# Optimization experiments

Measured on AMD Instinct MI355X. Metric: run time of the kernel, lower is better.

## Reference

```python
import jax, jax.numpy as jnp
import numpy as np

B, T, J, E, H = 32, 120, 24, 128, 8
d = E // H           # attention_dim = 16
D = J * E            # input_dim = 3072
FF = 256
NEG = -1e9


def _bn(x, g, b):
    # BatchNorm1d over channels-last layout: normalize each of D channels over (batch, time)
    m = x.mean(axis=(0, 1))
    v = x.var(axis=(0, 1))
    return (x - m) * jax.lax.rsqrt(v + 1e-5) * g + b


def setup_inputs() -> dict:
    key = jax.random.key(0)
    ks = jax.random.split(key, 12)
    s = 0.05  # keep activations well-scaled
    return {
        "src_seqs": jax.random.normal(ks[0], (B, T, D), jnp.float32),
        "Wq_t": jax.random.normal(ks[1], (H, J, d, E), jnp.float32) * s,
        "Wk_t": jax.random.normal(ks[2], (H, J, d, E), jnp.float32) * s,
        "Wv_t": jax.random.normal(ks[3], (H, J, d, E), jnp.float32) * s,
        "Wp_t": jax.random.normal(ks[4], (D, D), jnp.float32) * s,
        "bp_t": jnp.zeros((D,), jnp.float32),
        "g_t": jnp.ones((D,), jnp.float32),
        "b_t": jnp.zeros((D,), jnp.float32),
        "Wq_s": jax.random.normal(ks[5], (H, J, d, E), jnp.float32) * s,
        "Wk_s": jax.random.normal(ks[6], (H, d, E), jnp.float32) * s,
        "Wv_s": jax.random.normal(ks[7], (H, d, E), jnp.float32) * s,
        "Wp_s": jax.random.normal(ks[8], (D, D), jnp.float32) * s,
        "bp_s": jnp.zeros((D,), jnp.float32),
        "g_s": jnp.ones((D,), jnp.float32),
        "b_s": jnp.zeros((D,), jnp.float32),
        "W1": jax.random.normal(ks[9], (FF, D), jnp.float32) * s,
        "b1": jnp.zeros((FF,), jnp.float32),
        "W2": jax.random.normal(ks[10], (D, FF), jnp.float32) * s,
        "b2": jnp.zeros((D,), jnp.float32),
        "g_f": jnp.ones((D,), jnp.float32),
        "b_f": jnp.zeros((D,), jnp.float32),
    }


def reference(src_seqs, Wq_t, Wk_t, Wv_t, Wp_t, bp_t, g_t, b_t,
              Wq_s, Wk_s, Wv_s, Wp_s, bp_s, g_s, b_s,
              W1, b1, W2, b2, g_f, b_f):
    Bz, Tz, Dz = src_seqs.shape
    x = src_seqs.reshape(Bz, Tz, J, E)  # per-joint embeddings
    sc = 1.0 / jnp.sqrt(jnp.float32(d))

    # ---- temporal attention (per head h, per joint j; causal over time) ----
    q = jnp.einsum('btje,hjde->bhjtd', x, Wq_t)
    k = jnp.einsum('btje,hjde->bhjtd', x, Wk_t)
    v = jnp.einsum('btje,hjde->bhjtd', x, Wv_t)
    causal = jnp.where(jnp.tril(jnp.ones((Tz, Tz), bool)), 0.0, NEG)
    a = jax.nn.softmax(jnp.einsum('bhjtd,bhjsd->bhjts', q, k) * sc + causal, axis=-1)
    ta = jnp.einsum('bhjts,bhjsd->bhjtd', a, v)
    # concat order: heads outer, joints inner -> (b,t,h,j,d)
    ta = ta.transpose(0, 3, 1, 2, 4).reshape(Bz, Tz, Dz)
    ta = ta @ Wp_t.T + bp_t
    ta = _bn(ta + src_seqs, g_t, b_t)  # dropout=identity (eval)

    # ---- spatial attention (per head h; attends over joints, shared K/V proj) ----
    qs = jnp.einsum('btje,hjde->bhtjd', x, Wq_s)
    ks = jnp.einsum('btje,hde->bhtjd', x, Wk_s)
    vs = jnp.einsum('btje,hde->bhtjd', x, Wv_s)
    asft = jax.nn.softmax(jnp.einsum('bhtjd,bhtkd->bhtjk', qs, ks) * sc, axis=-1)
    sa = jnp.einsum('bhtjk,bhtkd->bhtjd', asft, vs)
    sa = sa.transpose(0, 2, 1, 3, 4).reshape(Bz, Tz, Dz)  # (b,t,h,j,d)
    sa = sa @ Wp_s.T + bp_s
    sa = _bn(sa + src_seqs, g_s, b_s)

    # ---- feed-forward + residual + norm ----
    att = ta + sa
    h1 = jax.nn.relu(att @ W1.T + b1)
    out = _bn((h1 @ W2.T + b2) + att, g_f, b_f)
    return out
```

## Files before the change

### kernel.cpp

```cpp
#include <hip/hip_runtime.h>

typedef unsigned short u16;
typedef __bf16 bf16x8 __attribute__((ext_vector_type(8)));
typedef float f4 __attribute__((ext_vector_type(4)));
typedef float float4v __attribute__((ext_vector_type(4)));
typedef u16 u16x4 __attribute__((ext_vector_type(4)));

#define NX 11796480
#define LDP 136

__device__ __forceinline__ float bf2f(u16 u){ __bf16 h = __builtin_bit_cast(__bf16, u); return (float)h; }
__device__ __forceinline__ u16 f2bf(float f){ __bf16 h = (__bf16)f; return __builtin_bit_cast(u16, h); }

__device__ __forceinline__ void gload_lds16(const u16* g, u16* l){
  __builtin_amdgcn_global_load_lds((const __attribute__((address_space(1))) void*)g,
                                   (__attribute__((address_space(3))) void*)l, 16, 0, 0);
}

__device__ __forceinline__ void cvt4seg(const float* __restrict__ in, u16* __restrict__ out, int i){
  float4v v = *(const float4v*)&in[i*4];
  u16x4 o;
  o[0]=f2bf(v[0]); o[1]=f2bf(v[1]); o[2]=f2bf(v[2]); o[3]=f2bf(v[3]);
  *(u16x4*)&out[i*4] = o;
}

__global__ void k_prep(const float* __restrict__ src, u16* __restrict__ x_bf,
                       const float* __restrict__ wpt, u16* __restrict__ wptb,
                       const float* __restrict__ wps, u16* __restrict__ wpsb,
                       const float* __restrict__ w1,  u16* __restrict__ w1b,
                       const float* __restrict__ w2,  u16* __restrict__ w2b,
                       const float* __restrict__ wqt, const float* __restrict__ wkt,
                       const float* __restrict__ wvt, const float* __restrict__ wqs,
                       const float* __restrict__ wks, const float* __restrict__ wvs,
                       u16* __restrict__ wcat, float* __restrict__ accs){
  int i = blockIdx.x*256 + threadIdx.x;
  if (i < 18432){ accs[i] = 0.f; return; }
  i -= 18432;
  if (i < 2949120){ cvt4seg(src, x_bf, i); return; }
  i -= 2949120;
  if (i < 2359296){ cvt4seg(wpt, wptb, i); return; }
  i -= 2359296;
  if (i < 2359296){ cvt4seg(wps, wpsb, i); return; }
  i -= 2359296;
  if (i < 196608){ cvt4seg(w1, w1b, i); return; }
  i -= 196608;
  if (i < 196608){ cvt4seg(w2, w2b, i); return; }
  i -= 196608;
  int e = i & 127;
  int n = (i >> 7) % 768;
  int j = i / (768*128);
  float v;
  if (n < 512){
    int tn = n >> 7, hh = (n >> 4) & 7, dd = n & 15;
    const float* W = (tn==0)? wqt : (tn==1)? wkt : (tn==2)? wvt : wqs;
    v = W[(((hh*24 + j)*16 + dd) << 7) + e];
  } else {
    int m = n - 512;
    int tn = m >> 7, hh = (m >> 4) & 7, dd = m & 15;
    const float* W = (tn==0)? wks : wvs;
    v = W[((hh*16 + dd) << 7) + e];
  }
  wcat[i] = f2bf(v);
}

__device__ __forceinline__ void gemm_tile(const u16* __restrict__ Ab, int lda,
                                          const u16* __restrict__ Bb, int ldb,
                                          int K, f4 acc[4][4], u16* As, u16* Bs)
{
  const int tid  = threadIdx.x;
  const int lane = tid & 63;
  const int wid  = tid >> 6;
  const int waveM = (wid >> 1) * 64;
  const int waveN = (wid & 1) * 64;
  const int quad = lane >> 4;
  const int r16  = lane & 15;
  const int srow = tid >> 3;
  const int gcol = ((tid & 7) ^ (srow & 7)) * 8;

  #pragma unroll
  for (int mt=0; mt<4; mt++)
    #pragma unroll
    for (int nt=0; nt<4; nt++)
      #pragma unroll
      for (int q=0; q<4; q++) acc[mt][nt][q] = 0.f;

  for (int k0 = 0; k0 < K; k0 += 64){
    __syncthreads();
    #pragma unroll
    for (int i=0; i<4; i++){
      int row = srow + i*32;
      gload_lds16(&Ab[(size_t)row*lda + k0 + gcol], As + wid*512 + i*2048);
      gload_lds16(&Bb[(size_t)row*ldb + k0 + gcol], Bs + wid*512 + i*2048);
    }
    __builtin_amdgcn_s_waitcnt(0);
    __syncthreads();
    #pragma unroll
    for (int kk=0; kk<2; kk++){
      bf16x8 af[4], bfr[4];
      const int soff = ((kk*4 + quad) ^ (r16 & 7)) * 8;
      #pragma unroll
      for (int mt=0; mt<4; mt++)
        af[mt] = *(const bf16x8*)&As[(waveM + mt*16 + r16)*64 + soff];
      #pragma unroll
      for (int nt=0; nt<4; nt++)
        bfr[nt] = *(const bf16x8*)&Bs[(waveN + nt*16 + r16)*64 + soff];
      #pragma unroll
      for (int mt=0; mt<4; mt++)
        #pragma unroll
        for (int nt=0; nt<4; nt++)
          acc[mt][nt] = __builtin_amdgcn_mfma_f32_16x16x32_bf16(af[mt], bfr[nt], acc[mt][nt], 0, 0, 0);
    }
  }
  __syncthreads();
}

__global__ __launch_bounds__(256)
void gemm_qkv(const u16* __restrict__ x, const u16* __restrict__ wcat,
              u16* __restrict__ qt, u16* __restrict__ kt, u16* __restrict__ vt,
              u16* __restrict__ qs, u16* __restrict__ ks, u16* __restrict__ vs)
{
  __shared__ __align__(16) u16 As[128*128];
  __shared__ __align__(16) u16 Bs[128*128];
  int m0 = blockIdx.x*128, j = blockIdx.y;
  const u16* Ab = x + (size_t)m0*3072 + j*128;
  const u16* Bbase = wcat + (size_t)j*98304;
  int tid = threadIdx.x, lane = tid & 63, wid = tid >> 6;
  int quad = lane >> 4, r16 = lane & 15;
  int srow16 = tid >> 4;
  int cslot  = tid & 15;
  int gcol   = (cslot ^ srow16) * 8;

  #pragma unroll
  for (int it=0; it<8; it++){
    int row = srow16 + it*16;
    gload_lds16(&Ab[(size_t)row*3072 + gcol], As + tid*8 + it*2048);
  }

  int waveM = (wid>>1)*64, waveN = (wid&1)*64;

  for (int nc=0; nc<6; nc++){
    const u16* Bb = Bbase + (size_t)(nc*128)*128;
    #pragma unroll
    for (int it=0; it<8; it++){
      int row = srow16 + it*16;
      gload_lds16(&Bb[(size_t)row*128 + gcol], Bs + tid*8 + it*2048);
    }
    __builtin_amdgcn_s_waitcnt(0);
    __syncthreads();

    f4 acc[4][4];
    #pragma unroll
    for (int mt=0; mt<4; mt++)
      #pragma unroll
      for (int nt=0; nt<4; nt++)
        #pragma unroll
        for (int q=0; q<4; q++) acc[mt][nt][q] = 0.f;

    #pragma unroll
    for (int kk=0; kk<4; kk++){
      bf16x8 af[4], bfr[4];
      const int soff = ((kk*4 + quad) ^ r16) * 8;
      #pragma unroll
      for (int mt=0; mt<4; mt++)
        af[mt] = *(const bf16x8*)&As[(waveM + mt*16 + r16)*128 + soff];
      #pragma unroll
      for (int nt=0; nt<4; nt++)
        bfr[nt] = *(const bf16x8*)&Bs[(waveN + nt*16 + r16)*128 + soff];
      #pragma unroll
      for (int mt=0; mt<4; mt++)
        #pragma unroll
        for (int nt=0; nt<4; nt++)
          acc[mt][nt] = __builtin_amdgcn_mfma_f32_16x16x32_bf16(af[mt], bfr[nt], acc[mt][nt], 0, 0, 0);
    }

    #pragma unroll
    for (int mt=0; mt<4; mt++){
      #pragma unroll
      for (int reg=0; reg<4; reg++){
        int row = m0 + waveM + mt*16 + quad*4 + reg;
        int b = row / 120, t = row % 120;
        #pragma unroll
        for (int nt=0; nt<4; nt++){
          int n = nc*128 + waveN + nt*16 + r16;
          u16 uv = f2bf(acc[mt][nt][reg]);
          if (n < 384){
            int tn = n >> 7, hh = (n >> 4) & 7, dd = n & 15;
            u16* base = (tn==0)? qt : (tn==1)? kt : vt;
            base[((((size_t)(b*8+hh)*24 + j)*120 + t) << 4) + dd] = uv;
          } else {
            int m2 = n - 384;
            int tn = m2 >> 7, hh = (m2 >> 4) & 7, dd = m2 & 15;
            u16* base = (tn==0)? qs : (tn==1)? ks : vs;
            base[((((size_t)row*8 + hh)*24 + j) << 4) + dd] = uv;
          }
        }
      }
    }
    __syncthreads();
  }
}


__device__ __forceinline__ void stageA384(const u16* __restrict__ g, int kcol,
                                          u16* __restrict__ slotA, int lane, int wid){
  #pragma unroll
  for (int i=0;i<2;i++){
    int row = wid*32 + i*16 + (lane>>2);
    int sw  = (((lane & 3) ^ ((lane>>3) & 3)) << 3);
    gload_lds16(&g[(size_t)row*3072 + kcol + sw], slotA + (wid*2+i)*512);
  }
}
__device__ __forceinline__ void stageB384(const u16* __restrict__ g, int kcol,
                                          u16* __restrict__ slotB, int lane, int wid){
  #pragma unroll
  for (int i=0;i<3;i++){
    int row = wid*48 + i*16 + (lane>>2);
    int sw  = (((lane & 3) ^ ((lane>>3) & 3)) << 3);
    gload_lds16(&g[(size_t)row*3072 + kcol + sw], slotB + (wid*3+i)*512);
  }
}

__global__ __launch_bounds__(512, 2)
void gemm_proj384(const u16* __restrict__ A0, const u16* __restrict__ B0, const float* __restrict__ b0,
                  const u16* __restrict__ A1, const u16* __restrict__ B1, const float* __restrict__ b1v,
                  const u16* __restrict__ resb, u16* __restrict__ O0, u16* __restrict__ O1,
                  float* __restrict__ st0, float* __restrict__ st1)
{
  __shared__ __align__(16) u16 smem[61440];
  const int tid = threadIdx.x, lane = tid & 63, wid = tid >> 6;
  const int quad = lane >> 4, r16 = lane & 15;
  const int wm = wid >> 2, wn = wid & 3;

  int lin = blockIdx.x + 15*blockIdx.y + 120*blockIdx.z;
  int nidx = (lin & 7)*30 + (lin >> 3);
  int zz = nidx / 120; int rem = nidx - zz*120;
  int by = rem / 15, bx = rem - by*15;

  const int m0 = bx*256, n0 = by*384;
  const u16* Ag = (zz ? A1 : A0) + (size_t)m0*3072;
  const u16* Bg = (zz ? B1 : B0) + (size_t)n0*3072;
  const float* bias = zz ? b1v : b0;
  u16* out = zz ? O1 : O0;
  float* stp = zz ? st1 : st0;

  const int soff = ((quad ^ ((r16>>1)&3)) << 3);
  const int arow = wm*128 + r16;
  const int brow = wn*96 + r16;

  f4 acc[8][6];
  #pragma unroll
  for (int i=0;i<8;i++)
    #pragma unroll
    for (int n=0;n<6;n++)
      #pragma unroll
      for (int q=0;q<4;q++) acc[i][n][q] = 0.f;

  u16* Sa = smem;
  u16* Sb = smem + 20480;
  u16* Sc = smem + 40960;

  stageA384(Ag, 0,  Sa,        lane, wid);
  stageB384(Bg, 0,  Sa + 8192, lane, wid);
  stageA384(Ag, 32, Sb,        lane, wid);
  stageB384(Bg, 32, Sb + 8192, lane, wid);
  asm volatile("s_waitcnt vmcnt(5)" ::: "memory");
  __builtin_amdgcn_s_barrier();

  const int NT = 96;
  bf16x8 af[4], bf[6];

  for (int t=0; t<NT; ++t){
    const int kc2 = ((t+2 < NT) ? (t+2) : 0) * 32;

    #pragma unroll
    for (int i=0;i<4;i++) af[i] = *(const bf16x8*)&Sa[(arow + i*16)*32 + soff];
    #pragma unroll
    for (int n=0;n<6;n++) bf[n] = *(const bf16x8*)&Sa[8192 + (brow + n*16)*32 + soff];
    stageA384(Ag, kc2, Sc, lane, wid);
    __builtin_amdgcn_s_setprio(1);
    #pragma unroll
    for (int i=0;i<4;i++)
      #pragma unroll
      for (int n=0;n<6;n++)
        acc[i][n] = __builtin_amdgcn_mfma_f32_16x16x32_bf16(af[i], bf[n], acc[i][n], 0,0,0);
    __builtin_amdgcn_s_setprio(0);

    #pragma unroll
    for (int i=0;i<4;i++) af[i] = *(const bf16x8*)&Sa[(arow + 64 + i*16)*32 + soff];
    stageB384(Bg, kc2, Sc + 8192, lane, wid);
    __builtin_amdgcn_s_setprio(1);
    #pragma unroll
    for (int i=0;i<4;i++)
      #pragma unroll
      for (int n=0;n<6;n++)
        acc[4+i][n] = __builtin_amdgcn_mfma_f32_16x16x32_bf16(af[i], bf[n], acc[4+i][n], 0,0,0);
    __builtin_amdgcn_s_setprio(0);

    asm volatile("s_waitcnt vmcnt(5)" ::: "memory");
    __builtin_amdgcn_s_barrier();
    u16* tp = Sa; Sa = Sb; Sb = Sc; Sc = tp;
  }
  asm volatile("s_waitcnt vmcnt(0)" ::: "memory");

  float bv[6];
  #pragma unroll
  for (int n=0;n<6;n++) bv[n] = bias[n0 + wn*96 + n*16 + r16];
  float s[6] = {0,0,0,0,0,0}, s2[6] = {0,0,0,0,0,0};
  #pragma unroll
  for (int mf=0; mf<8; mf++){
    #pragma unroll
    for (int reg=0; reg<4; reg++){
      int grow = m0 + wm*128 + mf*16 + quad*4 + reg;
      #pragma unroll
      for (int n=0;n<6;n++){
        int gcol = n0 + wn*96 + n*16 + r16;
        size_t idx = (size_t)grow*3072 + gcol;
        float v = acc[mf][n][reg] + bv[n] + bf2f(resb[idx]);
        out[idx] = f2bf(v);
        s[n] += v; s2[n] += v*v;
      }
    }
  }
  #pragma unroll
  for (int n=0;n<6;n++){
    float a = s[n], b = s2[n];
    a += __shfl_xor(a, 16); a += __shfl_xor(a, 32);
    b += __shfl_xor(b, 16); b += __shfl_xor(b, 32);
    if (quad == 0){
      int col = n0 + wn*96 + n*16 + r16;
      atomicAdd(&stp[col], a);
      atomicAdd(&stp[3072 + col], b);
    }
  }
}

__global__ __launch_bounds__(256)
void gemm_ff2(const u16* __restrict__ A, const u16* __restrict__ B, const float* __restrict__ bias,
              const u16* __restrict__ resb, u16* __restrict__ out, float* __restrict__ stp)
{
  __shared__ __align__(16) u16 As[128*64];
  __shared__ __align__(16) u16 Bs[128*64];
  int m0 = blockIdx.x*128, n0 = blockIdx.y*128;
  f4 acc[4][4];
  gemm_tile(A + (size_t)m0*256, 256, B + (size_t)n0*256, 256, 256, acc, As, Bs);
  int lane = threadIdx.x & 63, wid = threadIdx.x >> 6;
  int waveM = (wid>>1)*64, waveN = (wid&1)*64;
  int quad = lane>>4, r16 = lane&15;
  float s[4] = {0,0,0,0}, s2[4] = {0,0,0,0};
  #pragma unroll
  for (int mt=0; mt<4; mt++){
    #pragma unroll
    for (int reg=0; reg<4; reg++){
      int grow = m0 + waveM + mt*16 + quad*4 + reg;
      #pragma unroll
      for (int nt=0; nt<4; nt++){
        int gcol = n0 + waveN + nt*16 + r16;
        size_t idx = (size_t)grow*3072 + gcol;
        float v = acc[mt][nt][reg] + bias[gcol] + bf2f(resb[idx]);
        out[idx] = f2bf(v);
        s[nt] += v; s2[nt] += v*v;
      }
    }
  }
  #pragma unroll
  for (int nt=0; nt<4; nt++){
    float a = s[nt], b = s2[nt];
    a += __shfl_xor(a, 16); a += __shfl_xor(a, 32);
    b += __shfl_xor(b, 16); b += __shfl_xor(b, 32);
    if (quad == 0){
      int col = n0 + waveN + nt*16 + r16;
      atomicAdd(&stp[col], a);
      atomicAdd(&stp[3072 + col], b);
    }
  }
}

__device__ __forceinline__ void stageR_A(const u16* __restrict__ g, int kc, u16* __restrict__ slot,
                                         int tid, int srow, int gcol){
  gload_lds16(&g[(size_t)srow*3072 + kc + gcol], slot + tid*8);
}
__device__ __forceinline__ void stageR_B(const u16* __restrict__ g, int kc, u16* __restrict__ slot,
                                         int tid, int srow, int gcol){
  #pragma unroll
  for (int i=0;i<4;i++)
    gload_lds16(&g[(size_t)(srow + i*32)*3072 + kc + gcol], slot + 2048 + i*2048 + tid*8);
}

__global__ __launch_bounds__(256)
void gemm_relu(const u16* __restrict__ A, const u16* __restrict__ B,
               const float* __restrict__ bias, u16* __restrict__ out)
{
  __shared__ __align__(16) u16 smem[30720];
  const int tid = threadIdx.x, lane = tid & 63, wid = tid >> 6;
  const int quad = lane >> 4, r16 = lane & 15;
  const int waveM = (wid >> 1) * 16, waveN = (wid & 1) * 64;
  const int m0 = blockIdx.x * 32, n0 = blockIdx.y * 128;
  const u16* Ag = A + (size_t)m0 * 3072;
  const u16* Bg = B + (size_t)n0 * 3072;

  const int srow = tid >> 3;
  const int gcol = ((tid & 7) ^ (srow & 7)) * 8;

  f4 acc[4];
  #pragma unroll
  for (int n=0;n<4;n++)
    #pragma unroll
    for (int q=0;q<4;q++) acc[n][q] = 0.f;

  u16* Sa = smem;
  u16* Sb = smem + 10240;
  u16* Sc = smem + 20480;

  stageR_A(Ag, 0,  Sa, tid, srow, gcol);
  stageR_B(Bg, 0,  Sa, tid, srow, gcol);
  stageR_A(Ag, 64, Sb, tid, srow, gcol);
  stageR_B(Bg, 64, Sb, tid, srow, gcol);
  asm volatile("s_waitcnt vmcnt(5)" ::: "memory");
  __builtin_amdgcn_s_barrier();

  const int NT = 48;
  const int s0 = (quad ^ (r16 & 7)) * 8;
  const int s1 = ((4 + quad) ^ (r16 & 7)) * 8;

  for (int t=0; t<NT; ++t){
    const int kc2 = ((t+2 < NT) ? (t+2) : 0) * 64;

    bf16x8 a0 = *(const bf16x8*)&Sa[(waveM + r16)*64 + s0];
    bf16x8 b0[4];
    #pragma unroll
    for (int n=0;n<4;n++) b0[n] = *(const bf16x8*)&Sa[2048 + (waveN + n*16 + r16)*64 + s0];
    stageR_A(Ag, kc2, Sc, tid, srow, gcol);
    __builtin_amdgcn_s_setprio(1);
    #pragma unroll
    for (int n=0;n<4;n++)
      acc[n] = __builtin_amdgcn_mfma_f32_16x16x32_bf16(a0, b0[n], acc[n], 0,0,0);
    __builtin_amdgcn_s_setprio(0);

    bf16x8 a1 = *(const bf16x8*)&Sa[(waveM + r16)*64 + s1];
    bf16x8 b1[4];
    #pragma unroll
    for (int n=0;n<4;n++) b1[n] = *(const bf16x8*)&Sa[2048 + (waveN + n*16 + r16)*64 + s1];
    stageR_B(Bg, kc2, Sc, tid, srow, gcol);
    __builtin_amdgcn_s_setprio(1);
    #pragma unroll
    for (int n=0;n<4;n++)
      acc[n] = __builtin_amdgcn_mfma_f32_16x16x32_bf16(a1, b1[n], acc[n], 0,0,0);
    __builtin_amdgcn_s_setprio(0);

    asm volatile("s_waitcnt vmcnt(5)" ::: "memory");
    __builtin_amdgcn_s_barrier();
    u16* tp = Sa; Sa = Sb; Sb = Sc; Sc = tp;
  }
  asm volatile("s_waitcnt vmcnt(0)" ::: "memory");

  #pragma unroll
  for (int n=0;n<4;n++){
    int gcolo = n0 + waveN + n*16 + r16;
    float bv = bias[gcolo];
    #pragma unroll
    for (int reg=0; reg<4; reg++){
      int grow = m0 + waveM + quad*4 + reg;
      float v = acc[n][reg] + bv;
      out[(size_t)grow*256 + gcolo] = f2bf(v > 0.f ? v : 0.f);
    }
  }
}

__global__ __launch_bounds__(256)
void attn_both(const u16* __restrict__ qt, const u16* __restrict__ kt,
               const u16* __restrict__ vt, u16* __restrict__ ta,
               const u16* __restrict__ qsp, const u16* __restrict__ ksp,
               const u16* __restrict__ vsp, u16* __restrict__ sa)
{
  __shared__ __align__(16) char smem[39168];
  int tid = threadIdx.x, lane = tid & 63, wid = tid >> 6;
  int quad = lane >> 4, r16 = lane & 15;

  if (blockIdx.x < 6144){
    u16* P  = (u16*)smem;
    u16* Vt = (u16*)(smem + 34816);
    int blk = blockIdx.x;
    int b = blk / 192;
    int rem = blk % 192;
    int h = rem / 24, j = rem % 24;
    const u16* qb = qt + (size_t)blk*1920;
    const u16* kb = kt + (size_t)blk*1920;
    const u16* vb = vt + (size_t)blk*1920;

    if (tid < 240){
      int s = tid >> 1, hf = (tid & 1) * 8;
      bf16x8 vv = *(const bf16x8*)&vb[s*16 + hf];
      #pragma unroll
      for (int q=0;q<8;q++) Vt[(hf + q)*LDP + s] = __builtin_bit_cast(u16, (__bf16)vv[q]);
    }
    if (tid < 128){ int dd = tid >> 3, s = 120 + (tid & 7); Vt[dd*LDP + s] = 0; }
    __syncthreads();

    bf16x8 zv;
    #pragma unroll
    for (int i=0;i<8;i++) zv[i] = (__bf16)0.f;

    const int m0 = wid * 32;
    bf16x8 qf[2];
    #pragma unroll
    for (int mt=0; mt<2; mt++){
      int row = m0 + mt*16 + r16; if (row > 119) row = 119;
      qf[mt] = (quad < 2) ? *(const bf16x8*)&qb[row*16 + (quad&1)*8] : zv;
    }

    f4 S[2][8];
    #pragma unroll
    for (int nt=0; nt<8; nt++){
      int col = nt*16 + r16; int colc = col > 119 ? 119 : col;
      bf16x8 kf = (quad < 2) ? *(const bf16x8*)&kb[colc*16 + (quad&1)*8] : zv;
      #pragma unroll
      for (int mt=0; mt<2; mt++){
        f4 zz = {0.f, 0.f, 0.f, 0.f};
        S[mt][nt] = __builtin_amdgcn_mfma_f32_16x16x32_bf16(qf[mt], kf, zz, 0, 0, 0);
      }
    }

    #pragma unroll
    for (int mt=0; mt<2; mt++)
      #pragma unroll
      for (int nt=0; nt<8; nt++)
        #pragma unroll
        for (int reg=0; reg<4; reg++){
          int c = nt*16 + r16;
          int r = m0 + mt*16 + quad*4 + reg;
          float v = S[mt][nt][reg] * 0.25f;
          S[mt][nt][reg] = (c > r || c >= 120) ? -1e30f : v;
        }

    float Zr[2][4];
    #pragma unroll
    for (int mt=0; mt<2; mt++)
      #pragma unroll
      for (int reg=0; reg<4; reg++){
        float m = -1e30f;
        #pragma unroll
        for (int nt=0; nt<8; nt++) m = fmaxf(m, S[mt][nt][reg]);
        #pragma unroll
        for (int off=1; off<16; off<<=1) m = fmaxf(m, __shfl_xor(m, off, 16));
        float z = 0.f;
        #pragma unroll
        for (int nt=0; nt<8; nt++){
          float e = __expf(S[mt][nt][reg] - m);
          S[mt][nt][reg] = e;
          z += e;
        }
        #pragma unroll
        for (int off=1; off<16; off<<=1) z += __shfl_xor(z, off, 16);
        Zr[mt][reg] = z;
      }

    #pragma unroll
    for (int mt=0; mt<2; mt++)
      #pragma unroll
      for (int nt=0; nt<8; nt++)
        #pragma unroll
        for (int reg=0; reg<4; reg++)
          P[(m0 + mt*16 + quad*4 + reg)*LDP + nt*16 + r16] = f2bf(S[mt][nt][reg]);
    __syncthreads();

    f4 O[2];
    #pragma unroll
    for (int mt=0; mt<2; mt++){ O[mt][0]=0.f; O[mt][1]=0.f; O[mt][2]=0.f; O[mt][3]=0.f; }
    #pragma unroll
    for (int kt8=0; kt8<4; kt8++){
      bf16x8 vf = *(const bf16x8*)&Vt[r16*LDP + kt8*32 + quad*8];
      #pragma unroll
      for (int mt=0; mt<2; mt++){
        bf16x8 pf = *(const bf16x8*)&P[(m0 + mt*16 + r16)*LDP + kt8*32 + quad*8];
        O[mt] = __builtin_amdgcn_mfma_f32_16x16x32_bf16(pf, vf, O[mt], 0, 0, 0);
      }
    }

    #pragma unroll
    for (int mt=0; mt<2; mt++)
      #pragma unroll
      for (int reg=0; reg<4; reg++){
        int r = m0 + mt*16 + quad*4 + reg;
        if (r < 120){
          size_t idx = (size_t)(b*120 + r)*3072 + h*384 + j*16 + r16;
          ta[idx] = f2bf(O[mt][reg] / Zr[mt][reg]);
        }
      }
  } else {
    float* Ks = (float*)smem;
    float* Vs = (float*)(smem + 12288);
    int bt = blockIdx.x - 6144;
    size_t base = (size_t)bt * 3072;
    for (int c = tid; c < 384; c += 256){
      bf16x8 kv = *(const bf16x8*)&ksp[base + c*8];
      bf16x8 vv = *(const bf16x8*)&vsp[base + c*8];
      #pragma unroll
      for (int i=0;i<8;i++){ Ks[c*8+i] = (float)kv[i]; Vs[c*8+i] = (float)vv[i]; }
    }
    __syncthreads();
    if (tid < 192){
      int h = tid / 24, j = tid % 24;
      float q[16];
      #pragma unroll
      for (int d2=0; d2<16; d2++) q[d2] = bf2f(qsp[base + h*384 + j*16 + d2]);
      float sc[24], mx = -1e30f;
      #pragma unroll
      for (int kk=0; kk<24; kk++){
        float dot = 0.f;
        #pragma unroll
        for (int d2=0; d2<16; d2++) dot += q[d2]*Ks[h*384 + kk*16 + d2];
        sc[kk] = dot * 0.25f;
        mx = fmaxf(mx, sc[kk]);
      }
      float Z = 0.f, acc[16];
      #pragma unroll
      for (int d2=0; d2<16; d2++) acc[d2] = 0.f;
      #pragma unroll
      for (int kk=0; kk<24; kk++){
        float w = __expf(sc[kk] - mx);
        Z += w;
        #pragma unroll
        for (int d2=0; d2<16; d2++) acc[d2] += w*Vs[h*384 + kk*16 + d2];
      }
      float inv = 1.f / Z;
      #pragma unroll
      for (int d2=0; d2<16; d2++) sa[base + h*384 + j*16 + d2] = f2bf(acc[d2]*inv);
    }
  }
}

__global__ void bn_coef2(const float* __restrict__ accT, const float* __restrict__ gT,
                         const float* __restrict__ bT, float* __restrict__ cT,
                         const float* __restrict__ accS, const float* __restrict__ gS,
                         const float* __restrict__ bS, float* __restrict__ cS){
  int isS = blockIdx.x >= 12;
  const float* acc = isS ? accS : accT;
  const float* g   = isS ? gS : gT;
  const float* b   = isS ? bS : bT;
  float* coef      = isS ? cS : cT;
  int c = (blockIdx.x % 12)*256 + threadIdx.x;
  float mean = acc[c] * (1.f/3840.f);
  float var  = acc[3072+c] * (1.f/3840.f) - mean*mean;
  float sc = g[c] * rsqrtf(var + 1e-5f);
  coef[c] = sc;
  coef[3072+c] = b[c] - mean*sc;
}

__global__ void bn_coef(const float* __restrict__ acc, const float* __restrict__ g,
                        const float* __restrict__ b, float* __restrict__ coef){
  int c = blockIdx.x*256 + threadIdx.x;
  float mean = acc[c] * (1.f/3840.f);
  float var  = acc[3072+c] * (1.f/3840.f) - mean*mean;
  float sc = g[c] * rsqrtf(var + 1e-5f);
  coef[c] = sc;
  coef[3072+c] = b[c] - mean*sc;
}

__global__ void bn_apply2(const u16* __restrict__ Ytb, const u16* __restrict__ Ysb,
                          const float* __restrict__ ct, const float* __restrict__ cs,
                          u16* __restrict__ attB){
  int i = blockIdx.x*256 + threadIdx.x;
  int c = (i*4) % 3072;
  u16x4 yt = *(const u16x4*)&Ytb[i*4];
  u16x4 ys = *(const u16x4*)&Ysb[i*4];
  u16x4 o;
  #pragma unroll
  for (int k=0;k<4;k++){
    float a = bf2f(yt[k])*ct[c+k] + ct[3072+c+k] + bf2f(ys[k])*cs[c+k] + cs[3072+c+k];
    o[k] = f2bf(a);
  }
  *(u16x4*)&attB[i*4] = o;
}

__global__ void bn_out(const u16* __restrict__ Yfb, const float* __restrict__ cf,
                       float* __restrict__ out){
  int i = blockIdx.x*256 + threadIdx.x;
  int c = (i*4) % 3072;
  u16x4 yf = *(const u16x4*)&Yfb[i*4];
  float4v o;
  #pragma unroll
  for (int k=0;k<4;k++) o[k] = bf2f(yf[k])*cf[c+k] + cf[3072+c+k];
  *(float4v*)&out[i*4] = o;
}

extern "C" void kernel_launch(void* const* d_in, const int* in_sizes, int n_in,
                              void* d_out, int out_size, void* d_ws, size_t ws_size,
                              hipStream_t stream)
{
  const float* src  = (const float*)d_in[0];
  const float* Wq_t = (const float*)d_in[1];
  const float* Wk_t = (const float*)d_in[2];
  const float* Wv_t = (const float*)d_in[3];
  const float* Wp_t = (const float*)d_in[4];
  const float* bp_t = (const float*)d_in[5];
  const float* g_t  = (const float*)d_in[6];
  const float* b_t  = (const float*)d_in[7];
  const float* Wq_s = (const float*)d_in[8];
  const float* Wk_s = (const float*)d_in[9];
  const float* Wv_s = (const float*)d_in[10];
  const float* Wp_s = (const float*)d_in[11];
  const float* bp_s = (const float*)d_in[12];
  const float* g_s  = (const float*)d_in[13];
  const float* b_s  = (const float*)d_in[14];
  const float* W1   = (const float*)d_in[15];
  const float* b1   = (const float*)d_in[16];
  const float* W2   = (const float*)d_in[17];
  const float* b2   = (const float*)d_in[18];
  const float* g_f  = (const float*)d_in[19];
  const float* b_f  = (const float*)d_in[20];

  char* ws = (char*)d_ws;
  u16* x_bf  = (u16*)(ws + 0ull);
  u16* wptb  = (u16*)(ws + 23592960ull);
  u16* wpsb  = (u16*)(ws + 42467328ull);
  u16* w1b   = (u16*)(ws + 61341696ull);
  u16* w2b   = (u16*)(ws + 62914560ull);
  u16* wcat  = (u16*)(ws + 64487424ull);
  u16* qt    = (u16*)(ws + 69206016ull);
  u16* kt    = qt + NX;
  u16* vt    = kt + NX;
  u16* qs    = vt + NX;
  u16* ks    = qs + NX;
  u16* vs    = ks + NX;
  u16* tab   = (u16*)(ws + 210763776ull);
  u16* sab   = (u16*)(ws + 234356736ull);
  float* accT = (float*)(ws + 257949696ull);
  float* accS = accT + 6144;
  float* accF = accS + 6144;
  float* cT   = accF + 6144;
  float* cS   = cT + 6144;
  float* cF   = cS + 6144;
  u16* Ytb  = qt;
  u16* Ysb  = kt;
  u16* attB = vt;
  u16* Yfb  = qs;
  u16* h1   = wcat;
  float* out = (float*)d_out;

  k_prep<<<40776, 256, 0, stream>>>(src, x_bf, Wp_t, wptb, Wp_s, wpsb, W1, w1b, W2, w2b,
                                    Wq_t, Wk_t, Wv_t, Wq_s, Wk_s, Wv_s, wcat, accT);
  gemm_qkv<<<dim3(30,24), 256, 0, stream>>>(x_bf, wcat, qt, kt, vt, qs, ks, vs);
  attn_both<<<9984, 256, 0, stream>>>(qt, kt, vt, tab, qs, ks, vs, sab);
  gemm_proj384<<<dim3(15,8,2), 512, 0, stream>>>(tab, wptb, bp_t, sab, wpsb, bp_s,
                                                 x_bf, Ytb, Ysb, accT, accS);
  bn_coef2<<<24, 256, 0, stream>>>(accT, g_t, b_t, cT, accS, g_s, b_s, cS);
  bn_apply2<<<11520, 256, 0, stream>>>(Ytb, Ysb, cT, cS, attB);
  gemm_relu<<<dim3(120,2), 256, 0, stream>>>(attB, w1b, b1, h1);
  gemm_ff2<<<dim3(30,24), 256, 0, stream>>>(h1, w2b, b2, attB, Yfb, accF);
  bn_coef<<<12, 256, 0, stream>>>(accF, g_f, b_f, cF);
  bn_out<<<11520, 256, 0, stream>>>(Yfb, cF, out);
}
```

Measured before the change: 558.7 us.

## Double-buffer weight tiles in QKV and FF2 GEMMs, drop redundant attention barrier

gemm_qkv now splits the weight stream into 64-column chunks held in two LDS buffers. It prefetches chunk nc+2 while computing chunk nc, using partial vmcnt waits and raw s_barrier instead of a full wait each iteration. gemm_ff2 inlines its GEMM loop with double-buffered A/B K-tiles so global-to-LDS loads overlap MFMA work. A __syncthreads after writing P in the temporal attention kernel is removed, on the premise that each wave only reads the P rows it wrote. The aim is to hide load latency and cut barrier stalls, at the cost of smaller per-wave tiles in the QKV GEMM and reliance on correct vmcnt accounting.

Result: no change. 554.9 us (-0.7%).

```diff
diff --git a/kernel.cpp b/kernel.cpp
--- a/kernel.cpp
+++ b/kernel.cpp
@@ -63,55 +63,13 @@
   wcat[i] = f2bf(v);
 }
 
-__device__ __forceinline__ void gemm_tile(const u16* __restrict__ Ab, int lda,
-                                          const u16* __restrict__ Bb, int ldb,
-                                          int K, f4 acc[4][4], u16* As, u16* Bs)
-{
-  const int tid  = threadIdx.x;
-  const int lane = tid & 63;
-  const int wid  = tid >> 6;
-  const int waveM = (wid >> 1) * 64;
-  const int waveN = (wid & 1) * 64;
-  const int quad = lane >> 4;
-  const int r16  = lane & 15;
-  const int srow = tid >> 3;
-  const int gcol = ((tid & 7) ^ (srow & 7)) * 8;
-
-  #pragma unroll
-  for (int mt=0; mt<4; mt++)
-    #pragma unroll
-    for (int nt=0; nt<4; nt++)
-      #pragma unroll
-      for (int q=0; q<4; q++) acc[mt][nt][q] = 0.f;
-
-  for (int k0 = 0; k0 < K; k0 += 64){
-    __syncthreads();
-    #pragma unroll
-    for (int i=0; i<4; i++){
-      int row = srow + i*32;
-      gload_lds16(&Ab[(size_t)row*lda + k0 + gcol], As + wid*512 + i*2048);
-      gload_lds16(&Bb[(size_t)row*ldb + k0 + gcol], Bs + wid*512 + i*2048);
-    }
-    __builtin_amdgcn_s_waitcnt(0);
-    __syncthreads();
-    #pragma unroll
-    for (int kk=0; kk<2; kk++){
-      bf16x8 af[4], bfr[4];
-      const int soff = ((kk*4 + quad) ^ (r16 & 7)) * 8;
-      #pragma unroll
-      for (int mt=0; mt<4; mt++)
-        af[mt] = *(const bf16x8*)&As[(waveM + mt*16 + r16)*64 + soff];
-      #pragma unroll
-      for (int nt=0; nt<4; nt++)
-        bfr[nt] = *(const bf16x8*)&Bs[(waveN + nt*16 + r16)*64 + soff];
-      #pragma unroll
-      for (int mt=0; mt<4; mt++)
-        #pragma unroll
-        for (int nt=0; nt<4; nt++)
-          acc[mt][nt] = __builtin_amdgcn_mfma_f32_16x16x32_bf16(af[mt], bfr[nt], acc[mt][nt], 0, 0, 0);
-    }
-  }
-  __syncthreads();
+__device__ __forceinline__ void stageQB(const u16* __restrict__ Bb, u16* __restrict__ dst,
+                                        int tid, int srow16, int gcol){
+  #pragma unroll
+  for (int it=0; it<4; it++){
+    int row = srow16 + it*16;
+    gload_lds16(&Bb[(size_t)row*128 + gcol], dst + tid*8 + it*2048);
+  }
 }
 
 __global__ __launch_bounds__(256)
@@ -119,8 +77,10 @@
               u16* __restrict__ qt, u16* __restrict__ kt, u16* __restrict__ vt,
               u16* __restrict__ qs, u16* __restrict__ ks, u16* __restrict__ vs)
 {
-  __shared__ __align__(16) u16 As[128*128];
-  __shared__ __align__(16) u16 Bs[128*128];
+  __shared__ __align__(16) u16 smem[32768];
+  u16* As  = smem;
+  u16* Bs0 = smem + 16384;
+  u16* Bs1 = smem + 24576;
   int m0 = blockIdx.x*128, j = blockIdx.y;
   const u16* Ab = x + (size_t)m0*3072 + j*128;
   const u16* Bbase = wcat + (size_t)j*98304;
@@ -135,22 +95,17 @@
     int row = srow16 + it*16;
     gload_lds16(&Ab[(size_t)row*3072 + gcol], As + tid*8 + it*2048);
   }
-
-  int waveM = (wid>>1)*64, waveN = (wid&1)*64;
-
-  for (int nc=0; nc<6; nc++){
-    const u16* Bb = Bbase + (size_t)(nc*128)*128;
-    #pragma unroll
-    for (int it=0; it<8; it++){
-      int row = srow16 + it*16;
-      gload_lds16(&Bb[(size_t)row*128 + gcol], Bs + tid*8 + it*2048);
-    }
-    __builtin_amdgcn_s_waitcnt(0);
-    __syncthreads();
-
-    f4 acc[4][4];
-    #pragma unroll
-    for (int mt=0; mt<4; mt++)
+  stageQB(Bbase,            Bs0, tid, srow16, gcol);
+  stageQB(Bbase + 64*128,   Bs1, tid, srow16, gcol);
+  asm volatile("s_waitcnt vmcnt(4)" ::: "memory");
+  __builtin_amdgcn_s_barrier();
+
+  for (int nc=0; nc<12; nc++){
+    const u16* Bc = (nc & 1) ? Bs1 : Bs0;
+
+    f4 acc[2][4];
+    #pragma unroll
+    for (int mt=0; mt<2; mt++)
       #pragma unroll
       for (int nt=0; nt<4; nt++)
         #pragma unroll
@@ -158,30 +113,30 @@
 
     #pragma unroll
     for (int kk=0; kk<4; kk++){
-      bf16x8 af[4], bfr[4];
       const int soff = ((kk*4 + quad) ^ r16) * 8;
-      #pragma unroll
-      for (int mt=0; mt<4; mt++)
-        af[mt] = *(const bf16x8*)&As[(waveM + mt*16 + r16)*128 + soff];
+      bf16x8 af[2], bfr[4];
+      #pragma unroll
+      for (int mt=0; mt<2; mt++)
+        af[mt] = *(const bf16x8*)&As[(wid*32 + mt*16 + r16)*128 + soff];
       #pragma unroll
       for (int nt=0; nt<4; nt++)
-        bfr[nt] = *(const bf16x8*)&Bs[(waveN + nt*16 + r16)*128 + soff];
-      #pragma unroll
-      for (int mt=0; mt<4; mt++)
+        bfr[nt] = *(const bf16x8*)&Bc[(nt*16 + r16)*128 + soff];
+      #pragma unroll
+      for (int mt=0; mt<2; mt++)
         #pragma unroll
         for (int nt=0; nt<4; nt++)
           acc[mt][nt] = __builtin_amdgcn_mfma_f32_16x16x32_bf16(af[mt], bfr[nt], acc[mt][nt], 0, 0, 0);
     }
 
     #pragma unroll
-    for (int mt=0; mt<4; mt++){
+    for (int mt=0; mt<2; mt++){
       #pragma unroll
       for (int reg=0; reg<4; reg++){
-        int row = m0 + waveM + mt*16 + quad*4 + reg;
+        int row = m0 + wid*32 + mt*16 + quad*4 + reg;
         int b = row / 120, t = row % 120;
         #pragma unroll
         for (int nt=0; nt<4; nt++){
-          int n = nc*128 + waveN + nt*16 + r16;
+          int n = nc*64 + nt*16 + r16;
           u16 uv = f2bf(acc[mt][nt][reg]);
           if (n < 384){
             int tn = n >> 7, hh = (n >> 4) & 7, dd = n & 15;
@@ -196,10 +151,19 @@
         }
       }
     }
-    __syncthreads();
-  }
-}
-
+
+    if (nc < 11){
+      __builtin_amdgcn_s_barrier();
+      if (nc + 2 < 12){
+        stageQB(Bbase + (size_t)(nc+2)*64*128, (nc & 1) ? Bs1 : Bs0, tid, srow16, gcol);
+        asm volatile("s_waitcnt vmcnt(4)" ::: "memory");
+      } else {
+        asm volatile("s_waitcnt vmcnt(0)" ::: "memory");
+      }
+      __builtin_amdgcn_s_barrier();
+    }
+  }
+}
 
 __device__ __forceinline__ void stageA384(const u16* __restrict__ g, int kcol,
                                           u16* __restrict__ slotA, int lane, int wid){
@@ -334,18 +298,78 @@
   }
 }
 
+__device__ __forceinline__ void stageF(const u16* __restrict__ g, int k0,
+                                       u16* __restrict__ dst, int wid, int srow, int gcol){
+  #pragma unroll
+  for (int i=0;i<4;i++){
+    int row = srow + i*32;
+    gload_lds16(&g[(size_t)row*256 + k0 + gcol], dst + wid*512 + i*2048);
+  }
+}
+
 __global__ __launch_bounds__(256)
 void gemm_ff2(const u16* __restrict__ A, const u16* __restrict__ B, const float* __restrict__ bias,
               const u16* __restrict__ resb, u16* __restrict__ out, float* __restrict__ stp)
 {
-  __shared__ __align__(16) u16 As[128*64];
-  __shared__ __align__(16) u16 Bs[128*64];
+  __shared__ __align__(16) u16 smem[32768];
+  u16* Asb0 = smem;          u16* Asb1 = smem + 8192;
+  u16* Bsb0 = smem + 16384;  u16* Bsb1 = smem + 24576;
   int m0 = blockIdx.x*128, n0 = blockIdx.y*128;
+  const u16* Ag = A + (size_t)m0*256;
+  const u16* Bg = B + (size_t)n0*256;
+  int tid = threadIdx.x, lane = tid & 63, wid = tid >> 6;
+  int quad = lane>>4, r16 = lane&15;
+  int srow = tid >> 3;
+  int gcol = ((tid & 7) ^ (srow & 7)) * 8;
+  int waveM = (wid>>1)*64, waveN = (wid&1)*64;
+
   f4 acc[4][4];
-  gemm_tile(A + (size_t)m0*256, 256, B + (size_t)n0*256, 256, 256, acc, As, Bs);
-  int lane = threadIdx.x & 63, wid = threadIdx.x >> 6;
-  int waveM = (wid>>1)*64, waveN = (wid&1)*64;
-  int quad = lane>>4, r16 = lane&15;
+  #pragma unroll
+  for (int mt=0; mt<4; mt++)
+    #pragma unroll
+    for (int nt=0; nt<4; nt++)
+      #pragma unroll
+      for (int q=0; q<4; q++) acc[mt][nt][q] = 0.f;
+
+  stageF(Ag, 0,  Asb0, wid, srow, gcol);
+  stageF(Bg, 0,  Bsb0, wid, srow, gcol);
+  stageF(Ag, 64, Asb1, wid, srow, gcol);
+  stageF(Bg, 64, Bsb1, wid, srow, gcol);
+  asm volatile("s_waitcnt vmcnt(8)" ::: "memory");
+  __builtin_amdgcn_s_barrier();
+
+  for (int t=0; t<4; t++){
+    const u16* As = (t & 1) ? Asb1 : Asb0;
+    const u16* Bs = (t & 1) ? Bsb1 : Bsb0;
+    #pragma unroll
+    for (int kk=0; kk<2; kk++){
+      bf16x8 af[4], bfr[4];
+      const int soff = ((kk*4 + quad) ^ (r16 & 7)) * 8;
+      #pragma unroll
+      for (int mt=0; mt<4; mt++)
+        af[mt] = *(const bf16x8*)&As[(waveM + mt*16 + r16)*64 + soff];
+      #pragma unroll
+      for (int nt=0; nt<4; nt++)
+        bfr[nt] = *(const bf16x8*)&Bs[(waveN + nt*16 + r16)*64 + soff];
+      #pragma unroll
+      for (int mt=0; mt<4; mt++)
+        #pragma unroll
+        for (int nt=0; nt<4; nt++)
+          acc[mt][nt] = __builtin_amdgcn_mfma_f32_16x16x32_bf16(af[mt], bfr[nt], acc[mt][nt], 0, 0, 0);
+    }
+    if (t < 3){
+      __builtin_amdgcn_s_barrier();
+      if (t + 2 < 4){
+        stageF(Ag, (t+2)*64, (t & 1) ? Asb1 : Asb0, wid, srow, gcol);
+        stageF(Bg, (t+2)*64, (t & 1) ? Bsb1 : Bsb0, wid, srow, gcol);
+        asm volatile("s_waitcnt vmcnt(8)" ::: "memory");
+      } else {
+        asm volatile("s_waitcnt vmcnt(0)" ::: "memory");
+      }
+      __builtin_amdgcn_s_barrier();
+    }
+  }
+
   float s[4] = {0,0,0,0}, s2[4] = {0,0,0,0};
   #pragma unroll
   for (int mt=0; mt<4; mt++){
@@ -354,9 +378,9 @@
       int grow = m0 + waveM + mt*16 + quad*4 + reg;
       #pragma unroll
       for (int nt=0; nt<4; nt++){
-        int gcol = n0 + waveN + nt*16 + r16;
-        size_t idx = (size_t)grow*3072 + gcol;
-        float v = acc[mt][nt][reg] + bias[gcol] + bf2f(resb[idx]);
+        int gcolo = n0 + waveN + nt*16 + r16;
+        size_t idx = (size_t)grow*3072 + gcolo;
+        float v = acc[mt][nt][reg] + bias[gcolo] + bf2f(resb[idx]);
         out[idx] = f2bf(v);
         s[nt] += v; s2[nt] += v*v;
       }
@@ -561,7 +585,6 @@
         #pragma unroll
         for (int reg=0; reg<4; reg++)
           P[(m0 + mt*16 + quad*4 + reg)*LDP + nt*16 + r16] = f2bf(S[mt][nt][reg]);
-    __syncthreads();
 
     f4 O[2];
     #pragma unroll
```
